# Kernel tuning notes

Hardware: AMD Instinct MI355X
Metric: run time of the kernel (lower is better)

The kernel has to match this reference:

```python
import jax, jax.numpy as jnp
import numpy as np

GLOW_SIZE = 51
GLOW_SIGMA = 15.0


def _glow_kernel():
    # 1D gaussian, normalized, then outer product -> dense 51x51 kernel (as in torch module)
    grid = jnp.arange(GLOW_SIZE, dtype=jnp.float32) - GLOW_SIZE // 2
    g = jnp.exp(-grid ** 2 / (2.0 * GLOW_SIGMA * GLOW_SIGMA))
    g = g / g.sum()
    k2d = jnp.outer(g, g)  # [51, 51]
    # depthwise kernel OIHW with feature_group_count=3: [3, 1, 51, 51]
    return jnp.broadcast_to(k2d, (3, 1, GLOW_SIZE, GLOW_SIZE))


def setup_inputs() -> dict:
    key = jax.random.key(0)
    kx, = jax.random.split(key, 1)
    x = jax.random.uniform(kx, (8, 3, 1024, 1024), dtype=jnp.float32)  # images in [0,1]
    amount_param = jnp.zeros((), dtype=jnp.float32)  # nn.Parameter(torch.tensor(0.0))
    return {"x": x, "amount_param": amount_param}


def reference(x, amount_param):
    amount = jax.nn.sigmoid(amount_param) * 0.4  # 0.2 at init, so no early return
    kernel = _glow_kernel()
    pad = GLOW_SIZE // 2
    # per-channel (depthwise) 51x51 gaussian blur, same padding
    glow = jax.lax.conv_general_dilated(
        x, kernel,
        window_strides=(1, 1),
        padding=[(pad, pad), (pad, pad)],
        dimension_numbers=("NCHW", "OIHW", "NCHW"),
        feature_group_count=3,
    )
    glow = glow * 1.2
    # screen blend + clamp
    result = 1.0 - (1.0 - x) * (1.0 - glow * amount)
    return jnp.clip(result, 0.0, 1.0)
```

## Files before the change

### kernel.cpp

```cpp
#include <hip/hip_runtime.h>
#include <cmath>

#define HH 1024
#define WW 1024
#define KS 51
#define RAD 25
#define PLANE (HH * WW)

struct GaussW { float w[KS]; };

__global__ __launch_bounds__(256) void hblur_kernel(const float* __restrict__ x,
                                                    float* __restrict__ tmp,
                                                    GaussW gw)
{
    const int t    = threadIdx.x;
    const int lane = t & 63;
    const int r    = t >> 6;
    const long long row = (long long)blockIdx.x * 4 + r;
    const float* src = x + row * WW;
    const int j0 = lane * 16;

    float acc[16];
    #pragma unroll
    for (int d = 0; d < 16; d++) acc[d] = 0.f;

    #pragma unroll
    for (int i = 0; i < 18; i++) {
        const int b = j0 - 28 + i * 4;
        float4 v;
        if (b >= 0 && b + 3 < WW) {
            v = *(const float4*)(src + b);
        } else {
            float tv[4];
            #pragma unroll
            for (int q = 0; q < 4; q++) {
                const int c = b + q;
                tv[q] = (c >= 0 && c < WW) ? src[c] : 0.f;
            }
            v = make_float4(tv[0], tv[1], tv[2], tv[3]);
        }
        const float vq[4] = {v.x, v.y, v.z, v.w};
        #pragma unroll
        for (int q = 0; q < 4; q++) {
            const int wi = i * 4 + q;
            #pragma unroll
            for (int d = 0; d < 16; d++) {
                const int k = wi - 3 - d;
                if (k >= 0 && k < KS)
                    acc[d] = fmaf(gw.w[k], vq[q], acc[d]);
            }
        }
    }

    float* dst = tmp + row * WW;
    #pragma unroll
    for (int g = 0; g < 4; g++)
        *(float4*)(dst + j0 + g * 4) =
            make_float4(acc[g*4], acc[g*4+1], acc[g*4+2], acc[g*4+3]);
}

__global__ __launch_bounds__(256) void vblend_kernel(const float* __restrict__ tmp,
                                                     const float* __restrict__ x,
                                                     float* __restrict__ out,
                                                     GaussW gw,
                                                     const float* __restrict__ amountp)
{
    const int t      = threadIdx.x;
    const int bid    = blockIdx.x;
    const int plane  = bid >> 7;
    const int rem    = bid & 127;
    const int tile_x = rem >> 4;
    const int tile_y = rem & 15;
    const int c0     = tile_x * 128 + (t & 63) * 2;
    const int r0     = tile_y * 64 + (t >> 6) * 16;

    const float* tp = tmp + (size_t)plane * PLANE + c0;

    float2 acc[16];
    #pragma unroll
    for (int j = 0; j < 16; j++) acc[j] = make_float2(0.f, 0.f);

    #pragma unroll
    for (int i = 0; i < 66; i++) {
        const int ri = r0 - RAD + i;
        float2 v = make_float2(0.f, 0.f);
        if (ri >= 0 && ri < HH) v = *(const float2*)(tp + (size_t)ri * WW);
        #pragma unroll
        for (int j = 0; j < 16; j++) {
            const int k = i - j;
            if (k >= 0 && k < KS) {
                const float wk = gw.w[k];
                acc[j].x = fmaf(wk, v.x, acc[j].x);
                acc[j].y = fmaf(wk, v.y, acc[j].y);
            }
        }
    }

    const float p = amountp[0];
    const float s = 1.2f * (0.4f / (1.f + expf(-p)));

    const float* xp = x   + (size_t)plane * PLANE + c0;
    float*       op = out + (size_t)plane * PLANE + c0;
    #pragma unroll
    for (int j = 0; j < 16; j++) {
        const float2 xv = *(const float2*)(xp + (size_t)(r0 + j) * WW);
        float2 res;
        res.x = 1.f - (1.f - xv.x) * (1.f - s * acc[j].x);
        res.y = 1.f - (1.f - xv.y) * (1.f - s * acc[j].y);
        res.x = fminf(fmaxf(res.x, 0.f), 1.f);
        res.y = fminf(fmaxf(res.y, 0.f), 1.f);
        *(float2*)(op + (size_t)(r0 + j) * WW) = res;
    }
}

extern "C" void kernel_launch(void* const* d_in, const int* in_sizes, int n_in,
                              void* d_out, int out_size, void* d_ws, size_t ws_size,
                              hipStream_t stream)
{
    const float* x       = (const float*)d_in[0];
    const float* amountp = (const float*)d_in[1];
    float* out = (float*)d_out;
    float* tmp = (float*)d_ws;

    GaussW gw;
    {
        double e[KS], sum = 0.0;
        for (int i = 0; i < KS; i++) {
            const double d = (double)(i - RAD);
            e[i] = exp(-d * d / (2.0 * 15.0 * 15.0));
            sum += e[i];
        }
        for (int i = 0; i < KS; i++) gw.w[i] = (float)(e[i] / sum);
    }

    const int total_planes = in_sizes[0] / PLANE;
    const size_t plane_bytes = (size_t)PLANE * sizeof(float);
    int P = (int)(ws_size / plane_bytes);
    if (P < 1) P = 1;
    if (P > total_planes) P = total_planes;

    for (int p0 = 0; p0 < total_planes; p0 += P) {
        const int pc = (total_planes - p0 < P) ? (total_planes - p0) : P;
        hblur_kernel<<<pc * 256, 256, 0, stream>>>(x + (size_t)p0 * PLANE, tmp, gw);
        vblend_kernel<<<pc * 128, 256, 0, stream>>>(tmp,
                                                    x + (size_t)p0 * PLANE,
                                                    out + (size_t)p0 * PLANE,
                                                    gw, amountp);
    }
}
```

Before: 295.4 us.

## Stage vertical-blur tile in LDS and shrink per-thread horizontal outputs

The horizontal pass now gives each thread 4 outputs instead of 16, with one row per block, so there are more threads. The vertical pass first loads a 178x64 tile of the intermediate into shared memory and then computes 128 rows per block in two 16-row passes per thread. Before, each thread read its 66-row halo straight from global memory. The change trades global halo re-reads for LDS reads, at the cost of more redundant horizontal loads (15 float4 loads for 4 outputs) and lower occupancy from the roughly 45KB of shared memory per block.

```diff
diff --git a/kernel.cpp b/kernel.cpp
--- a/kernel.cpp
+++ b/kernel.cpp
@@ -6,6 +6,8 @@
 #define KS 51
 #define RAD 25
 #define PLANE (HH * WW)
+#define TROWS 128
+#define LROWS (TROWS + KS - 1)
 
 struct GaussW { float w[KS]; };
 
@@ -15,48 +17,41 @@
 {
     const int t    = threadIdx.x;
     const int lane = t & 63;
-    const int r    = t >> 6;
-    const long long row = (long long)blockIdx.x * 4 + r;
+    const int seg  = t >> 6;
+    const long long row = blockIdx.x;
     const float* src = x + row * WW;
-    const int j0 = lane * 16;
+    const int c = seg * 256 + lane * 4;
 
-    float acc[16];
-    #pragma unroll
-    for (int d = 0; d < 16; d++) acc[d] = 0.f;
+    float acc[4] = {0.f, 0.f, 0.f, 0.f};
 
     #pragma unroll
-    for (int i = 0; i < 18; i++) {
-        const int b = j0 - 28 + i * 4;
+    for (int q = 0; q < 15; q++) {
+        const int b = c - 28 + q * 4;
         float4 v;
-        if (b >= 0 && b + 3 < WW) {
+        if (b >= 0 && b <= WW - 4) {
             v = *(const float4*)(src + b);
         } else {
             float tv[4];
             #pragma unroll
-            for (int q = 0; q < 4; q++) {
-                const int c = b + q;
-                tv[q] = (c >= 0 && c < WW) ? src[c] : 0.f;
+            for (int e = 0; e < 4; e++) {
+                const int cc = b + e;
+                tv[e] = (cc >= 0 && cc < WW) ? src[cc] : 0.f;
             }
             v = make_float4(tv[0], tv[1], tv[2], tv[3]);
         }
-        const float vq[4] = {v.x, v.y, v.z, v.w};
+        const float ve[4] = {v.x, v.y, v.z, v.w};
         #pragma unroll
-        for (int q = 0; q < 4; q++) {
-            const int wi = i * 4 + q;
+        for (int e = 0; e < 4; e++) {
             #pragma unroll
-            for (int d = 0; d < 16; d++) {
-                const int k = wi - 3 - d;
+            for (int d = 0; d < 4; d++) {
+                const int k = q * 4 + e - 3 - d;
                 if (k >= 0 && k < KS)
-                    acc[d] = fmaf(gw.w[k], vq[q], acc[d]);
+                    acc[d] = fmaf(gw.w[k], ve[e], acc[d]);
             }
         }
     }
 
-    float* dst = tmp + row * WW;
-    #pragma unroll
-    for (int g = 0; g < 4; g++)
-        *(float4*)(dst + j0 + g * 4) =
-            make_float4(acc[g*4], acc[g*4+1], acc[g*4+2], acc[g*4+3]);
+    *(float4*)(tmp + row * WW + c) = make_float4(acc[0], acc[1], acc[2], acc[3]);
 }
 
 __global__ __launch_bounds__(256) void vblend_kernel(const float* __restrict__ tmp,
@@ -65,51 +60,65 @@
                                                      GaussW gw,
                                                      const float* __restrict__ amountp)
 {
+    __shared__ float ht[LROWS * 64];
     const int t      = threadIdx.x;
     const int bid    = blockIdx.x;
     const int plane  = bid >> 7;
     const int rem    = bid & 127;
-    const int tile_x = rem >> 4;
-    const int tile_y = rem & 15;
-    const int c0     = tile_x * 128 + (t & 63) * 2;
-    const int r0     = tile_y * 64 + (t >> 6) * 16;
-
-    const float* tp = tmp + (size_t)plane * PLANE + c0;
-
-    float2 acc[16];
-    #pragma unroll
-    for (int j = 0; j < 16; j++) acc[j] = make_float2(0.f, 0.f);
+    const int tile_x = rem >> 3;
+    const int tile_y = rem & 7;
+    const int c0     = tile_x * 64;
+    const int r0     = tile_y * TROWS;
+    const float* tp  = tmp + (size_t)plane * PLANE;
 
     #pragma unroll
-    for (int i = 0; i < 66; i++) {
-        const int ri = r0 - RAD + i;
-        float2 v = make_float2(0.f, 0.f);
-        if (ri >= 0 && ri < HH) v = *(const float2*)(tp + (size_t)ri * WW);
-        #pragma unroll
-        for (int j = 0; j < 16; j++) {
-            const int k = i - j;
-            if (k >= 0 && k < KS) {
-                const float wk = gw.w[k];
-                acc[j].x = fmaf(wk, v.x, acc[j].x);
-                acc[j].y = fmaf(wk, v.y, acc[j].y);
-            }
+    for (int i = 0; i < 12; i++) {
+        const int idx = i * 256 + t;
+        if (idx < LROWS * 16) {
+            const int lr = idx >> 4;
+            const int cf = idx & 15;
+            const int gr = r0 - RAD + lr;
+            float4 v = make_float4(0.f, 0.f, 0.f, 0.f);
+            if (gr >= 0 && gr < HH)
+                v = *(const float4*)(tp + (size_t)gr * WW + c0 + cf * 4);
+            *(float4*)(&ht[lr * 64 + cf * 4]) = v;
         }
     }
+    __syncthreads();
 
     const float p = amountp[0];
     const float s = 1.2f * (0.4f / (1.f + expf(-p)));
 
-    const float* xp = x   + (size_t)plane * PLANE + c0;
-    float*       op = out + (size_t)plane * PLANE + c0;
+    const int col = t & 63;
+    const int rg  = t >> 6;
+    const float* xp = x   + (size_t)plane * PLANE + c0 + col;
+    float*       op = out + (size_t)plane * PLANE + c0 + col;
+
     #pragma unroll
-    for (int j = 0; j < 16; j++) {
-        const float2 xv = *(const float2*)(xp + (size_t)(r0 + j) * WW);
-        float2 res;
-        res.x = 1.f - (1.f - xv.x) * (1.f - s * acc[j].x);
-        res.y = 1.f - (1.f - xv.y) * (1.f - s * acc[j].y);
-        res.x = fminf(fmaxf(res.x, 0.f), 1.f);
-        res.y = fminf(fmaxf(res.y, 0.f), 1.f);
-        *(float2*)(op + (size_t)(r0 + j) * WW) = res;
+    for (int pass = 0; pass < 2; pass++) {
+        const int lr0 = rg * 32 + pass * 16;
+        float acc[16];
+        #pragma unroll
+        for (int j = 0; j < 16; j++) acc[j] = 0.f;
+
+        #pragma unroll
+        for (int i = 0; i < 66; i++) {
+            const float v = ht[(lr0 + i) * 64 + col];
+            #pragma unroll
+            for (int j = 0; j < 16; j++) {
+                const int k = i - j;
+                if (k >= 0 && k < KS)
+                    acc[j] = fmaf(gw.w[k], v, acc[j]);
+            }
+        }
+
+        #pragma unroll
+        for (int j = 0; j < 16; j++) {
+            const size_t off = (size_t)(r0 + lr0 + j) * WW;
+            const float xv = xp[off];
+            float res = 1.f - (1.f - xv) * (1.f - s * acc[j]);
+            op[off] = fminf(fmaxf(res, 0.f), 1.f);
+        }
     }
 }
 
@@ -141,7 +150,7 @@
 
     for (int p0 = 0; p0 < total_planes; p0 += P) {
         const int pc = (total_planes - p0 < P) ? (total_planes - p0) : P;
-        hblur_kernel<<<pc * 256, 256, 0, stream>>>(x + (size_t)p0 * PLANE, tmp, gw);
+        hblur_kernel<<<pc * 1024, 256, 0, stream>>>(x + (size_t)p0 * PLANE, tmp, gw);
         vblend_kernel<<<pc * 128, 256, 0, stream>>>(tmp,
                                                     x + (size_t)p0 * PLANE,
                                                     out + (size_t)p0 * PLANE,
```

Result: slower. 327.7 us (+10.9%).
